# Optimization experiments

Measured on AMD Instinct MI355X. Metric: run time of the kernel, lower is better.

## Reference

```python
import jax, jax.numpy as jnp
import numpy as np

INF = 1e38  # matches torch source constant


def setup_inputs() -> dict:
    key = jax.random.key(0)
    k1, k2, k3 = jax.random.split(key, 3)
    B, N, D = 16, 2048, 512
    query = jax.random.normal(k1, (B, N, D), dtype=jnp.float32)
    # nn.Linear(dims, dims, bias=False): weight [out, in] = [D, D]
    W_in = jax.random.normal(k2, (D, D), dtype=jnp.float32) * (1.0 / np.sqrt(D))
    # nn.Linear(2*dims, dims, bias=False): weight [D, 2D]
    W_out = jax.random.normal(k3, (D, 2 * D), dtype=jnp.float32) * (1.0 / np.sqrt(2 * D))
    return {"query": query, "W_in": W_in, "W_out": W_out}


def reference(query, W_in, W_out):
    B, N, D = query.shape
    # linear_in: y = x @ W^T
    q = jnp.einsum("bnd,ed->bne", query, W_in)  # [B, N, D]
    # full QK^T scores
    scores = jnp.einsum("bnd,bmd->bnm", q, q)  # [B, N, N]
    # torch: scores[:, triu_mask] = -INF  -> mask upper triangle INCLUDING diagonal
    mask = jnp.triu(jnp.ones((N, N), dtype=bool))
    scores = jnp.where(mask, -INF, scores)
    weights = jax.nn.softmax(scores, axis=-1)
    # row 0 is all -INF -> softmax gives uniform; torch zeroes it explicitly
    weights = weights.at[:, 0, :].set(0.0)
    mix = jnp.einsum("bnm,bmd->bnd", weights, q)  # [B, N, D]
    combined = jnp.concatenate([mix, q], axis=-1)  # [B, N, 2D]
    # linear_out (no activation since activation=None)
    output = jnp.einsum("bnc,dc->bnd", combined, W_out)  # [B, N, D]
    return output
```

## Files before the change

kernel.cpp:

```cpp
#include <hip/hip_runtime.h>

typedef _Float16 f16;
typedef _Float16 half8 __attribute__((ext_vector_type(8)));
typedef _Float16 half4 __attribute__((ext_vector_type(4)));
typedef float floatx4 __attribute__((ext_vector_type(4)));

#define MFMA16(a, b, c) __builtin_amdgcn_mfma_f32_16x16x32_f16(a, b, c, 0, 0, 0)

union H8 { half8 v; f16 e[8]; };

__device__ __forceinline__ void gload16(const void* g, void* l) {
    __builtin_amdgcn_global_load_lds((const __attribute__((address_space(1))) void*)g,
                                     (__attribute__((address_space(3))) void*)l, 16, 0, 0);
}

__global__ __launch_bounds__(256) void k_cvt(const float* __restrict__ query,
                                             const float* __restrict__ Wi,
                                             const float* __restrict__ Wo,
                                             f16* __restrict__ q16,
                                             f16* __restrict__ W16)
{
    int i = blockIdx.x * 256 + threadIdx.x;
    const float4* src;
    f16* dst;
    if (i < 4194304) { src = (const float4*)query + i; dst = q16 + (size_t)i * 4; }
    else if (i < 4259840) { int j = i - 4194304; src = (const float4*)Wi + j; dst = W16 + (size_t)j * 4; }
    else { int j = i - 4259840; src = (const float4*)Wo + j; dst = W16 + 262144 + (size_t)j * 4; }
    float4 v = *src;
    half4 h = {(f16)v.x, (f16)v.y, (f16)v.z, (f16)v.w};
    *reinterpret_cast<half4*>(dst) = h;
}

__global__ __launch_bounds__(256) void k_qin(const f16* __restrict__ q16,
                                             const f16* __restrict__ W16,
                                             f16* __restrict__ comb,
                                             f16* __restrict__ qT)
{
    __shared__ char sm[34816];
    f16* At = (f16*)sm;
    f16* Bt = (f16*)(sm + 16384);
    const int tid = threadIdx.x, lane = tid & 63, w = tid >> 6;
    const int l15 = lane & 15, quad = lane >> 4;
    const int id = blockIdx.x, xcd = id & 7, u = id >> 3;
    const int mbase = (xcd * 32 + (u >> 2)) * 128;
    const int nbase = (u & 3) * 128;
    const int wm = (w & 1) * 64, wn = (w >> 1) * 64;
    const int ia = wm >> 4, jb = wn >> 4;

    floatx4 acc[4][4];
#pragma unroll
    for (int i = 0; i < 4; ++i)
#pragma unroll
        for (int j = 0; j < 4; ++j) acc[i][j] = (floatx4)0.f;

    for (int k0 = 0; k0 < 512; k0 += 64) {
        __syncthreads();
#pragma unroll
        for (int jr = 0; jr < 4; ++jr) {
            int bi = jr * 4 + w, i2 = bi >> 1, s = bi & 1;
            gload16(q16 + (size_t)(mbase + i2 * 16 + l15) * 512 + k0 + s * 32 + quad * 8, At + bi * 512);
            gload16(W16 + (size_t)(nbase + i2 * 16 + l15) * 512 + k0 + s * 32 + quad * 8, Bt + bi * 512);
        }
        __syncthreads();
#pragma unroll
        for (int s = 0; s < 2; ++s) {
            half8 a[4], bf[4];
#pragma unroll
            for (int i = 0; i < 4; ++i)
                a[i] = *reinterpret_cast<half8*>(At + ((ia + i) * 2 + s) * 512 + lane * 8);
#pragma unroll
            for (int j = 0; j < 4; ++j)
                bf[j] = *reinterpret_cast<half8*>(Bt + ((jb + j) * 2 + s) * 512 + lane * 8);
#pragma unroll
            for (int i = 0; i < 4; ++i)
#pragma unroll
                for (int j = 0; j < 4; ++j)
                    acc[i][j] = MFMA16(a[i], bf[j], acc[i][j]);
        }
    }
    const int bb = mbase >> 11, tb = mbase & 2047;
    f16* ct = (f16*)sm;
    __syncthreads();
#pragma unroll
    for (int i = 0; i < 4; ++i)
#pragma unroll
        for (int j = 0; j < 4; ++j)
#pragma unroll
            for (int r = 0; r < 4; ++r)
                ct[(wm + i * 16 + quad * 4 + r) * 136 + wn + j * 16 + l15] = (f16)acc[i][j][r];
    __syncthreads();
#pragma unroll
    for (int it = 0; it < 8; ++it) {
        int c = it * 256 + tid, r = c >> 4, c8 = (c & 15) << 3;
        *reinterpret_cast<half8*>(comb + (size_t)(mbase + r) * 1024 + 512 + nbase + c8) =
            *reinterpret_cast<half8*>(ct + r * 136 + c8);
    }
    __syncthreads();
#pragma unroll
    for (int i = 0; i < 4; ++i)
#pragma unroll
        for (int j = 0; j < 4; ++j) {
            half4 h = {(f16)acc[i][j][0], (f16)acc[i][j][1], (f16)acc[i][j][2], (f16)acc[i][j][3]};
            *reinterpret_cast<half4*>(ct + (wn + j * 16 + l15) * 136 + wm + i * 16 + quad * 4) = h;
        }
    __syncthreads();
#pragma unroll
    for (int it = 0; it < 8; ++it) {
        int c = it * 256 + tid, dd = c >> 4, tc = (c & 15) << 3;
        *reinterpret_cast<half8*>(qT + ((size_t)bb * 512 + nbase + dd) * 2048 + tb + tc) =
            *reinterpret_cast<half8*>(ct + dd * 136 + tc);
    }
}

__global__ __launch_bounds__(256) void k_sgemm(const f16* __restrict__ comb,
                                               float* __restrict__ Sg, int batch0)
{
    __shared__ char sm[32768];
    f16* At = (f16*)sm;
    f16* Bt = (f16*)(sm + 16384);
    const int tid = threadIdx.x, lane = tid & 63, w = tid >> 6;
    const int l15 = lane & 15, quad = lane >> 4;
    const int wm = (w & 1) * 64, wn = (w >> 1) * 64;
    const int ia = wm >> 4, jb = wn >> 4;

    int bx = blockIdx.x, mt = 0;
    while ((mt + 1) * (mt + 2) / 2 <= bx) ++mt;
    const int nt = bx - mt * (mt + 1) / 2;
    const int b = batch0 + blockIdx.y;
    const f16* qa = comb + ((size_t)b * 2048 + mt * 128) * 1024 + 512;
    const f16* qb = comb + ((size_t)b * 2048 + nt * 128) * 1024 + 512;

    floatx4 acc[4][4];
#pragma unroll
    for (int i = 0; i < 4; ++i)
#pragma unroll
        for (int j = 0; j < 4; ++j) acc[i][j] = (floatx4)0.f;

    for (int k0 = 0; k0 < 512; k0 += 64) {
        __syncthreads();
#pragma unroll
        for (int jr = 0; jr < 4; ++jr) {
            int bi = jr * 4 + w, i2 = bi >> 1, s = bi & 1;
            gload16(qa + (size_t)(i2 * 16 + l15) * 1024 + k0 + s * 32 + quad * 8, At + bi * 512);
            gload16(qb + (size_t)(i2 * 16 + l15) * 1024 + k0 + s * 32 + quad * 8, Bt + bi * 512);
        }
        __syncthreads();
#pragma unroll
        for (int s = 0; s < 2; ++s) {
            half8 a[4], bf[4];
#pragma unroll
            for (int i = 0; i < 4; ++i)
                a[i] = *reinterpret_cast<half8*>(At + ((ia + i) * 2 + s) * 512 + lane * 8);
#pragma unroll
            for (int j = 0; j < 4; ++j)
                bf[j] = *reinterpret_cast<half8*>(Bt + ((jb + j) * 2 + s) * 512 + lane * 8);
#pragma unroll
            for (int i = 0; i < 4; ++i)
#pragma unroll
                for (int j = 0; j < 4; ++j)
                    acc[i][j] = MFMA16(a[i], bf[j], acc[i][j]);
        }
    }
    float* St = Sg + ((size_t)blockIdx.y * 136 + bx) * 16384;
#pragma unroll
    for (int i = 0; i < 4; ++i)
#pragma unroll
        for (int j = 0; j < 4; ++j)
#pragma unroll
            for (int r = 0; r < 4; ++r)
                St[(wm + i * 16 + quad * 4 + r) * 128 + wn + j * 16 + l15] = acc[i][j][r];
}

__global__ __launch_bounds__(256) void k_softmax(float* Sg)
{
    const int tid = threadIdx.x, lane = tid & 63, w = tid >> 6;
    const int row = blockIdx.x * 4 + w;
    const int gb = blockIdx.y;
    const int mt = row >> 7;
    const size_t tbase = ((size_t)gb * 136 + (size_t)(mt * (mt + 1)) / 2) * 16384;
    const int padlen = (mt + 1) * 128;
    const int r128 = (row & 127) * 128;
    f16* Ph = (f16*)Sg;

    float sv[32];
    float m = -1e38f;
#pragma unroll
    for (int it = 0; it < 32; ++it) {
        int c = it * 64 + lane;
        float p = -1e38f;
        if (c < row) {
            p = Sg[tbase + (size_t)(c >> 7) * 16384 + r128 + (c & 127)];
            m = fmaxf(m, p);
        }
        sv[it] = p;
    }
#pragma unroll
    for (int msk = 32; msk >= 1; msk >>= 1) m = fmaxf(m, __shfl_xor(m, msk));
    float l = 0.f;
#pragma unroll
    for (int it = 0; it < 32; ++it) {
        int c = it * 64 + lane;
        float p = 0.f;
        if (c < row) { p = __expf(sv[it] - m); l += p; }
        sv[it] = p;
    }
#pragma unroll
    for (int msk = 32; msk >= 1; msk >>= 1) l += __shfl_xor(l, msk);
    const float invl = (row > 0) ? 1.f / l : 0.f;
#pragma unroll
    for (int it = 0; it < 32; ++it) {
        int c = it * 64 + lane;
        if (c < padlen)
            Ph[2 * (tbase + (size_t)(c >> 7) * 16384 + r128) + (c & 127)] = (f16)(sv[it] * invl);
    }
}

__global__ __launch_bounds__(256) void k_pv(const float* Sg,
                                            const f16* __restrict__ qT,
                                            f16* __restrict__ comb, int batch0)
{
    __shared__ char sm[65536];
    const int tid = threadIdx.x, lane = tid & 63, w = tid >> 6;
    const int l15 = lane & 15, quad = lane >> 4;
    const int wm = (w & 1) * 64, wn = (w >> 1) * 64;
    const int ia = wm >> 4, jb = wn >> 4;
    const int id = blockIdx.x;
    const int p = id & 7, nb = (id >> 3) & 3, gb = id >> 5;
    const int b = batch0 + gb;
    const f16* Ph = (const f16*)(Sg + (size_t)gb * 136 * 16384);
    const f16* qTb = qT + ((size_t)b * 512 + nb * 128) * 2048;

    for (int t = 0; t < 2; ++t) {
        const int mt = t ? (15 - p) : p;
        const int tb0 = mt * (mt + 1) / 2;
        const int kit = (mt + 1) * 2;

        floatx4 acc[4][4];
#pragma unroll
        for (int i = 0; i < 4; ++i)
#pragma unroll
            for (int j = 0; j < 4; ++j) acc[i][j] = (floatx4)0.f;

        auto STAGE = [&](int it, int bsel) {
            f16* At = (f16*)(sm + bsel * 32768);
            f16* Bt = At + 8192;
            const int k0 = it * 64;
            const int tt = tb0 + (k0 >> 7), c0 = k0 & 64;
#pragma unroll
            for (int jr = 0; jr < 4; ++jr) {
                int bi = jr * 4 + w, i2 = bi >> 1, s = bi & 1;
                gload16(Ph + 2 * ((size_t)tt * 16384 + (size_t)(i2 * 16 + l15) * 128) + c0 + s * 32 + quad * 8,
                        At + bi * 512);
                gload16(qTb + (size_t)(i2 * 16 + l15) * 2048 + k0 + s * 32 + quad * 8, Bt + bi * 512);
            }
        };

        STAGE(0, 0);
        __syncthreads();
        for (int it = 0; it < kit; ++it) {
            const int cur = it & 1;
            if (it + 1 < kit) STAGE(it + 1, cur ^ 1);
            f16* At = (f16*)(sm + cur * 32768);
            f16* Bt = At + 8192;
#pragma unroll
            for (int s = 0; s < 2; ++s) {
                half8 a[4], bf[4];
#pragma unroll
                for (int i = 0; i < 4; ++i)
                    a[i] = *reinterpret_cast<half8*>(At + ((ia + i) * 2 + s) * 512 + lane * 8);
#pragma unroll
                for (int j = 0; j < 4; ++j)
                    bf[j] = *reinterpret_cast<half8*>(Bt + ((jb + j) * 2 + s) * 512 + lane * 8);
#pragma unroll
                for (int i = 0; i < 4; ++i)
#pragma unroll
                    for (int j = 0; j < 4; ++j)
                        acc[i][j] = MFMA16(a[i], bf[j], acc[i][j]);
            }
            __syncthreads();
        }

        f16* ct = (f16*)sm;
#pragma unroll
        for (int i = 0; i < 4; ++i)
#pragma unroll
            for (int j = 0; j < 4; ++j)
#pragma unroll
                for (int r = 0; r < 4; ++r)
                    ct[(wm + i * 16 + quad * 4 + r) * 136 + wn + j * 16 + l15] = (f16)acc[i][j][r];
        __syncthreads();
#pragma unroll
        for (int it = 0; it < 8; ++it) {
            int c = it * 256 + tid, r = c >> 4, c8 = (c & 15) << 3;
            *reinterpret_cast<half8*>(comb + ((size_t)b * 2048 + mt * 128 + r) * 1024 + nb * 128 + c8) =
                *reinterpret_cast<half8*>(ct + r * 136 + c8);
        }
        __syncthreads();
    }
}

__global__ __launch_bounds__(256) void k_out(const f16* __restrict__ comb,
                                             const f16* __restrict__ Wo16,
                                             float* __restrict__ out)
{
    __shared__ char sm[32768];
    f16* At = (f16*)sm;
    f16* Bt = (f16*)(sm + 16384);
    const int tid = threadIdx.x, lane = tid & 63, w = tid >> 6;
    const int l15 = lane & 15, quad = lane >> 4;
    const int id = blockIdx.x, xcd = id & 7, u = id >> 3;
    const int mbase = (xcd * 32 + (u >> 2)) * 128;
    const int nbase = (u & 3) * 128;
    const int wm = (w & 1) * 64, wn = (w >> 1) * 64;
    const int ia = wm >> 4, jb = wn >> 4;

    floatx4 acc[4][4];
#pragma unroll
    for (int i = 0; i < 4; ++i)
#pragma unroll
        for (int j = 0; j < 4; ++j) acc[i][j] = (floatx4)0.f;

    for (int k0 = 0; k0 < 1024; k0 += 64) {
        __syncthreads();
#pragma unroll
        for (int jr = 0; jr < 4; ++jr) {
            int bi = jr * 4 + w, i2 = bi >> 1, s = bi & 1;
            gload16(comb + (size_t)(mbase + i2 * 16 + l15) * 1024 + k0 + s * 32 + quad * 8,
                    At + bi * 512);
            gload16(Wo16 + (size_t)(nbase + i2 * 16 + l15) * 1024 + k0 + s * 32 + quad * 8,
                    Bt + bi * 512);
        }
        __syncthreads();
#pragma unroll
        for (int s = 0; s < 2; ++s) {
            half8 a[4], bf[4];
#pragma unroll
            for (int i = 0; i < 4; ++i)
                a[i] = *reinterpret_cast<half8*>(At + ((ia + i) * 2 + s) * 512 + lane * 8);
#pragma unroll
            for (int j = 0; j < 4; ++j)
                bf[j] = *reinterpret_cast<half8*>(Bt + ((jb + j) * 2 + s) * 512 + lane * 8);
#pragma unroll
            for (int i = 0; i < 4; ++i)
#pragma unroll
                for (int j = 0; j < 4; ++j)
                    acc[i][j] = MFMA16(a[i], bf[j], acc[i][j]);
        }
    }
#pragma unroll
    for (int i = 0; i < 4; ++i)
#pragma unroll
        for (int j = 0; j < 4; ++j)
#pragma unroll
            for (int r = 0; r < 4; ++r)
                out[(size_t)(mbase + wm + i * 16 + quad * 4 + r) * 512 + nbase + wn + j * 16 + l15] =
                    acc[i][j][r];
}

extern "C" void kernel_launch(void* const* d_in, const int* in_sizes, int n_in,
                              void* d_out, int out_size, void* d_ws, size_t ws_size,
                              hipStream_t stream)
{
    const float* query = (const float*)d_in[0];
    const float* W_in  = (const float*)d_in[1];
    const float* W_out = (const float*)d_in[2];
    float* out = (float*)d_out;

    const size_t XOFF = 102236160ull;
    f16* comb = (f16*)d_ws;
    f16* qT   = comb + (size_t)32768 * 1024;
    f16* W16  = qT + (size_t)16 * 512 * 2048;
    f16* q16  = (f16*)((char*)d_ws + XOFF);
    const size_t sgb = 136ull * 16384 * 4;
    int ng;
    if (ws_size >= XOFF + 16 * sgb)      ng = 16;
    else if (ws_size >= XOFF + 8 * sgb)  ng = 8;
    else                                 ng = 4;
    float* Sg = (float*)((char*)d_ws + XOFF);

    k_cvt<<<17152, 256, 0, stream>>>(query, W_in, W_out, q16, W16);
    k_qin<<<1024, 256, 0, stream>>>(q16, W16, comb, qT);
    for (int g = 0; g < 16 / ng; ++g) {
        k_sgemm<<<dim3(136, ng), 256, 0, stream>>>(comb, Sg, g * ng);
        k_softmax<<<dim3(512, ng), 256, 0, stream>>>(Sg);
        k_pv<<<32 * ng, 256, 0, stream>>>(Sg, qT, comb, g * ng);
    }
    k_out<<<1024, 256, 0, stream>>>(comb, W16 + 262144, out);
}
```

Before: 436.9 us.

## Double-buffer LDS tiles in the input, score and output GEMM kernels

The three tiled GEMM kernels (input projection, QK^T scores, output projection) now split shared memory into two 32KB stages. Each iteration issues the asynchronous global-to-LDS load for the next K tile before running the MFMAs on the current tile, with one barrier per iteration instead of two. The aim is to hide global load latency behind matrix math. In exchange, LDS per block grows to 64KB, which can cut how many blocks fit on a CU.

```diff
diff --git a/kernel.cpp b/kernel.cpp
--- a/kernel.cpp
+++ b/kernel.cpp
@@ -36,9 +36,7 @@
                                              f16* __restrict__ comb,
                                              f16* __restrict__ qT)
 {
-    __shared__ char sm[34816];
-    f16* At = (f16*)sm;
-    f16* Bt = (f16*)(sm + 16384);
+    __shared__ char sm[65536];
     const int tid = threadIdx.x, lane = tid & 63, w = tid >> 6;
     const int l15 = lane & 15, quad = lane >> 4;
     const int id = blockIdx.x, xcd = id & 7, u = id >> 3;
@@ -53,15 +51,24 @@
 #pragma unroll
         for (int j = 0; j < 4; ++j) acc[i][j] = (floatx4)0.f;
 
-    for (int k0 = 0; k0 < 512; k0 += 64) {
-        __syncthreads();
+    auto STAGE = [&](int k0, int bsel) {
+        f16* At = (f16*)(sm + bsel * 32768);
+        f16* Bt = At + 8192;
 #pragma unroll
         for (int jr = 0; jr < 4; ++jr) {
             int bi = jr * 4 + w, i2 = bi >> 1, s = bi & 1;
             gload16(q16 + (size_t)(mbase + i2 * 16 + l15) * 512 + k0 + s * 32 + quad * 8, At + bi * 512);
             gload16(W16 + (size_t)(nbase + i2 * 16 + l15) * 512 + k0 + s * 32 + quad * 8, Bt + bi * 512);
         }
-        __syncthreads();
+    };
+
+    STAGE(0, 0);
+    __syncthreads();
+    for (int it = 0; it < 8; ++it) {
+        const int cur = it & 1;
+        if (it < 7) STAGE((it + 1) * 64, cur ^ 1);
+        f16* At = (f16*)(sm + cur * 32768);
+        f16* Bt = At + 8192;
 #pragma unroll
         for (int s = 0; s < 2; ++s) {
             half8 a[4], bf[4];
@@ -77,10 +84,10 @@
                 for (int j = 0; j < 4; ++j)
                     acc[i][j] = MFMA16(a[i], bf[j], acc[i][j]);
         }
+        __syncthreads();
     }
     const int bb = mbase >> 11, tb = mbase & 2047;
     f16* ct = (f16*)sm;
-    __syncthreads();
 #pragma unroll
     for (int i = 0; i < 4; ++i)
 #pragma unroll
@@ -115,9 +122,7 @@
 __global__ __launch_bounds__(256) void k_sgemm(const f16* __restrict__ comb,
                                                float* __restrict__ Sg, int batch0)
 {
-    __shared__ char sm[32768];
-    f16* At = (f16*)sm;
-    f16* Bt = (f16*)(sm + 16384);
+    __shared__ char sm[65536];
     const int tid = threadIdx.x, lane = tid & 63, w = tid >> 6;
     const int l15 = lane & 15, quad = lane >> 4;
     const int wm = (w & 1) * 64, wn = (w >> 1) * 64;
@@ -136,15 +141,24 @@
 #pragma unroll
         for (int j = 0; j < 4; ++j) acc[i][j] = (floatx4)0.f;
 
-    for (int k0 = 0; k0 < 512; k0 += 64) {
-        __syncthreads();
+    auto STAGE = [&](int k0, int bsel) {
+        f16* At = (f16*)(sm + bsel * 32768);
+        f16* Bt = At + 8192;
 #pragma unroll
         for (int jr = 0; jr < 4; ++jr) {
             int bi = jr * 4 + w, i2 = bi >> 1, s = bi & 1;
             gload16(qa + (size_t)(i2 * 16 + l15) * 1024 + k0 + s * 32 + quad * 8, At + bi * 512);
             gload16(qb + (size_t)(i2 * 16 + l15) * 1024 + k0 + s * 32 + quad * 8, Bt + bi * 512);
         }
-        __syncthreads();
+    };
+
+    STAGE(0, 0);
+    __syncthreads();
+    for (int it = 0; it < 8; ++it) {
+        const int cur = it & 1;
+        if (it < 7) STAGE((it + 1) * 64, cur ^ 1);
+        f16* At = (f16*)(sm + cur * 32768);
+        f16* Bt = At + 8192;
 #pragma unroll
         for (int s = 0; s < 2; ++s) {
             half8 a[4], bf[4];
@@ -160,6 +174,7 @@
                 for (int j = 0; j < 4; ++j)
                     acc[i][j] = MFMA16(a[i], bf[j], acc[i][j]);
         }
+        __syncthreads();
     }
     float* St = Sg + ((size_t)blockIdx.y * 136 + bx) * 16384;
 #pragma unroll
@@ -303,9 +318,7 @@
                                              const f16* __restrict__ Wo16,
                                              float* __restrict__ out)
 {
-    __shared__ char sm[32768];
-    f16* At = (f16*)sm;
-    f16* Bt = (f16*)(sm + 16384);
+    __shared__ char sm[65536];
     const int tid = threadIdx.x, lane = tid & 63, w = tid >> 6;
     const int l15 = lane & 15, quad = lane >> 4;
     const int id = blockIdx.x, xcd = id & 7, u = id >> 3;
@@ -320,8 +333,9 @@
 #pragma unroll
         for (int j = 0; j < 4; ++j) acc[i][j] = (floatx4)0.f;
 
-    for (int k0 = 0; k0 < 1024; k0 += 64) {
-        __syncthreads();
+    auto STAGE = [&](int k0, int bsel) {
+        f16* At = (f16*)(sm + bsel * 32768);
+        f16* Bt = At + 8192;
 #pragma unroll
         for (int jr = 0; jr < 4; ++jr) {
             int bi = jr * 4 + w, i2 = bi >> 1, s = bi & 1;
@@ -330,7 +344,15 @@
             gload16(Wo16 + (size_t)(nbase + i2 * 16 + l15) * 1024 + k0 + s * 32 + quad * 8,
                     Bt + bi * 512);
         }
-        __syncthreads();
+    };
+
+    STAGE(0, 0);
+    __syncthreads();
+    for (int it = 0; it < 16; ++it) {
+        const int cur = it & 1;
+        if (it < 15) STAGE((it + 1) * 64, cur ^ 1);
+        f16* At = (f16*)(sm + cur * 32768);
+        f16* Bt = At + 8192;
 #pragma unroll
         for (int s = 0; s < 2; ++s) {
             half8 a[4], bf[4];
@@ -346,6 +368,7 @@
                 for (int j = 0; j < 4; ++j)
                     acc[i][j] = MFMA16(a[i], bf[j], acc[i][j]);
         }
+        __syncthreads();
     }
 #pragma unroll
     for (int i = 0; i < 4; ++i)
```

Result: no change. 432.0 us (-1.1%).
